# Kernel optimization log

Measured on AMD Instinct MI355X. Metric: run time of the kernel, lower is better.

## Reference

```python
import jax, jax.numpy as jnp
import numpy as np

N_NODES = 500000
N_EDGES = 5000000
EMBD = 16
BN_EPS = 1e-5


def setup_inputs() -> dict:
    key = jax.random.key(0)
    ks = jax.random.split(key, 16)
    d = EMBD
    s = 0.25  # param scale ~ 1/sqrt(d)
    inp = {
        "x": jax.random.normal(ks[0], (N_NODES, d), jnp.float32),
        "edge_index": jax.random.randint(ks[1], (2, N_EDGES), 0, N_NODES, jnp.int64 if jax.config.jax_enable_x64 else jnp.int32),
        "edge_attr": jax.random.normal(ks[2], (N_EDGES, d), jnp.float32),
        # ResGatedGraphConv params (torch Linear math: y = x @ W + b, W stored (in,out))
        "Wk": jax.random.normal(ks[3], (d, d), jnp.float32) * s,
        "bk": jax.random.normal(ks[4], (d,), jnp.float32) * s,
        "Wq": jax.random.normal(ks[5], (d, d), jnp.float32) * s,
        "bq": jax.random.normal(ks[6], (d,), jnp.float32) * s,
        "Wv": jax.random.normal(ks[7], (d, d), jnp.float32) * s,
        "bv": jax.random.normal(ks[8], (d,), jnp.float32) * s,
        "We": jax.random.normal(ks[9], (d, d), jnp.float32) * s,   # lin_edge, no bias
        "Ws": jax.random.normal(ks[10], (d, d), jnp.float32) * s,  # lin_skip (root weight)
        "bs": jax.random.normal(ks[11], (d,), jnp.float32) * s,
        "bias": jax.random.normal(ks[12], (d,), jnp.float32) * s,  # conv output bias
        # BatchNorm1d affine params
        "gamma": jnp.ones((d,), jnp.float32),
        "beta": jnp.zeros((d,), jnp.float32),
    }
    return inp


def reference(x, edge_index, edge_attr, Wk, bk, Wq, bq, Wv, bv, We, Ws, bs, bias, gamma, beta):
    # --- ResGatedGraphConv (PyG semantics, act=sigmoid, root_weight=True) ---
    src = edge_index[0]  # j (source)
    tgt = edge_index[1]  # i (target, aggregation index)
    k = x @ Wk + bk      # lin_key(x_i side)   [N, d]
    q = x @ Wq + bq      # lin_query(x_j side) [N, d]
    v = x @ Wv + bv      # lin_value(x_j side) [N, d]
    e = edge_attr @ We   # lin_edge (bias=False) [E, d]
    # message: sigmoid(k_i + e_ij + q_j) * v_j
    gate = jax.nn.sigmoid(k[tgt] + e + q[src])
    msg = gate * v[src]  # [E, d]
    agg = jax.ops.segment_sum(msg, tgt, num_segments=N_NODES)  # scatter-add to targets
    h = agg + (x @ Ws + bs) + bias  # root skip + conv bias
    # --- BatchNorm1d (training mode: batch statistics over node dim) ---
    mean = jnp.mean(h, axis=0)
    var = jnp.mean(jnp.square(h - mean), axis=0)  # biased variance
    h = (h - mean) * jax.lax.rsqrt(var + BN_EPS) * gamma + beta
    # --- ReLU + residual ---
    h = jax.nn.relu(h)
    return x + h
```

## Files before the change

### kernel.cpp

```cpp
#include <hip/hip_runtime.h>
#include <hip/hip_bf16.h>
#include <hip/hip_fp16.h>

#define D 16

typedef _Float16 f16x4 __attribute__((ext_vector_type(4)));
typedef float f32x4 __attribute__((ext_vector_type(4)));

__global__ void node_prep(const float* __restrict__ x,
                          const float* __restrict__ Wk, const float* __restrict__ bk,
                          const float* __restrict__ Wq, const float* __restrict__ bq,
                          const float* __restrict__ Wv, const float* __restrict__ bv,
                          const float* __restrict__ Ws, const float* __restrict__ bs,
                          const float* __restrict__ bias,
                          __half* __restrict__ k_h, __half* __restrict__ qv_h,
                          float* __restrict__ skip, int n_nodes) {
    __shared__ float sWk[D * D], sWq[D * D], sWv[D * D], sWs[D * D], sb[4 * D];
    for (int i = threadIdx.x; i < D * D; i += blockDim.x) {
        sWk[i] = Wk[i]; sWq[i] = Wq[i]; sWv[i] = Wv[i]; sWs[i] = Ws[i];
    }
    if (threadIdx.x < D) {
        sb[threadIdx.x]         = bk[threadIdx.x];
        sb[D + threadIdx.x]     = bq[threadIdx.x];
        sb[2 * D + threadIdx.x] = bv[threadIdx.x];
        sb[3 * D + threadIdx.x] = bs[threadIdx.x] + bias[threadIdx.x];
    }
    __syncthreads();
    int n = blockIdx.x * blockDim.x + threadIdx.x;
    if (n >= n_nodes) return;

    float xr[D];
    const float4* xp = (const float4*)(x + (size_t)n * D);
#pragma unroll
    for (int i = 0; i < 4; i++) {
        float4 t = xp[i];
        xr[4*i] = t.x; xr[4*i+1] = t.y; xr[4*i+2] = t.z; xr[4*i+3] = t.w;
    }
    float kr[D], qr[D], vr[D], hr[D];
#pragma unroll
    for (int c = 0; c < D; c++) {
        kr[c] = sb[c]; qr[c] = sb[D + c]; vr[c] = sb[2*D + c]; hr[c] = sb[3*D + c];
    }
#pragma unroll
    for (int j = 0; j < D; j++) {
        float xj = xr[j];
#pragma unroll
        for (int c = 0; c < D; c++) {
            kr[c] = fmaf(xj, sWk[j * D + c], kr[c]);
            qr[c] = fmaf(xj, sWq[j * D + c], qr[c]);
            vr[c] = fmaf(xj, sWv[j * D + c], vr[c]);
            hr[c] = fmaf(xj, sWs[j * D + c], hr[c]);
        }
    }
    __align__(16) __half2 kp[8];
#pragma unroll
    for (int i = 0; i < 8; i++) kp[i] = __floats2half2_rn(kr[2*i], kr[2*i+1]);
    float4* kd = (float4*)(k_h + (size_t)n * D);
    kd[0] = *(float4*)&kp[0];
    kd[1] = *(float4*)&kp[4];
    __align__(16) __half2 qp[16];
#pragma unroll
    for (int i = 0; i < 8; i++) qp[i]     = __floats2half2_rn(qr[2*i], qr[2*i+1]);
#pragma unroll
    for (int i = 0; i < 8; i++) qp[8 + i] = __floats2half2_rn(vr[2*i], vr[2*i+1]);
    float4* qd = (float4*)(qv_h + (size_t)n * 32);
#pragma unroll
    for (int i = 0; i < 4; i++) qd[i] = *(float4*)&qp[4*i];
    float4* sp = (float4*)(skip + (size_t)n * D);
#pragma unroll
    for (int i = 0; i < 4; i++)
        sp[i] = make_float4(hr[4*i], hr[4*i+1], hr[4*i+2], hr[4*i+3]);
}

__global__ void edge_msg_mfma(const int* __restrict__ ei, const float* __restrict__ ea,
                              const float* __restrict__ We,
                              const __half* __restrict__ k_h,
                              const __half* __restrict__ qv_h,
                              __half* __restrict__ hagg,
                              int n_edges) {
    __shared__ __align__(16) int ssrc[64];
    __shared__ __align__(16) int stgt[64];
    int lane = threadIdx.x & 63;
    int wv = threadIdx.x >> 6;
    int c = lane & 15;
    int g = lane >> 4;

    f16x4 bfrag;
#pragma unroll
    for (int i = 0; i < 4; i++) bfrag[i] = (_Float16)We[(4*g + i) * D + c];

    long long blockbase = (long long)blockIdx.x * 64;
    {
        int t = threadIdx.x;
        if (t < 64) {
            long long e = blockbase + t;
            ssrc[t] = (e < n_edges) ? __builtin_nontemporal_load(&ei[e]) : 0;
        } else if (t < 128) {
            long long e = blockbase + (t - 64);
            stgt[t - 64] = (e < n_edges) ? __builtin_nontemporal_load(&ei[(size_t)n_edges + e]) : 0;
        }
    }
    __syncthreads();

    long long wbase = blockbase + (long long)wv * 16;
    if (wbase >= n_edges) return;

    long long arow = wbase + c;
    if (arow >= n_edges) arow = n_edges - 1;
    const float* ap = ea + (size_t)arow * D + 4 * g;
    float av0 = __builtin_nontemporal_load(ap + 0);
    float av1 = __builtin_nontemporal_load(ap + 1);
    float av2 = __builtin_nontemporal_load(ap + 2);
    float av3 = __builtin_nontemporal_load(ap + 3);
    f16x4 afrag = { (_Float16)av0, (_Float16)av1, (_Float16)av2, (_Float16)av3 };

    f32x4 e4 = __builtin_amdgcn_mfma_f32_16x16x16f16(afrag, bfrag, (f32x4){0.f,0.f,0.f,0.f}, 0, 0, 0);

    int le = wv * 16 + 4 * g;
    int4 src4 = *(const int4*)(ssrc + le);
    int4 tgt4 = *(const int4*)(stgt + le);
    int srcs[4] = { src4.x, src4.y, src4.z, src4.w };
    int tgts[4] = { tgt4.x, tgt4.y, tgt4.z, tgt4.w };

    float msg[4];
#pragma unroll
    for (int r = 0; r < 4; r++) {
        float kk = __half2float(k_h[(size_t)tgts[r] * D + c]);
        float qq = __half2float(qv_h[(size_t)srcs[r] * 32 + c]);
        float vv = __half2float(qv_h[(size_t)srcs[r] * 32 + D + c]);
        float z = kk + e4[r] + qq;
        msg[r] = vv / (1.f + __expf(-z));
    }

#pragma unroll
    for (int r = 0; r < 4; r++) {
        float partner = __shfl_xor(msg[r], 1);
        long long eidx = wbase + 4 * g + r;
        if (((c & 1) == 0) && eidx < n_edges) {
            __half2 m2 = __floats2half2_rn(msg[r], partner);
            unsafeAtomicAdd((__half2*)&hagg[(size_t)tgts[r] * D + c], m2);
        }
    }
}

__global__ void bn_stats(const float* __restrict__ skip, const __half* __restrict__ hagg,
                         float* __restrict__ stats, int n_nodes) {
    float s = 0.f, ss = 0.f;
    size_t total = (size_t)n_nodes * D;
    size_t stride = (size_t)gridDim.x * blockDim.x;
    for (size_t i = (size_t)blockIdx.x * blockDim.x + threadIdx.x; i < total; i += stride) {
        float val = skip[i] + __half2float(hagg[i]);
        s += val;
        ss = fmaf(val, val, ss);
    }
    s += __shfl_xor(s, 16); s += __shfl_xor(s, 32);
    ss += __shfl_xor(ss, 16); ss += __shfl_xor(ss, 32);
    __shared__ float ls[4 * D], lss[4 * D];
    int wave = threadIdx.x >> 6, lane = threadIdx.x & 63;
    if (lane < D) { ls[wave * D + lane] = s; lss[wave * D + lane] = ss; }
    __syncthreads();
    if (threadIdx.x < D) {
        float ts = 0.f, tss = 0.f;
#pragma unroll
        for (int w = 0; w < 4; w++) { ts += ls[w * D + threadIdx.x]; tss += lss[w * D + threadIdx.x]; }
        atomicAdd(&stats[threadIdx.x], ts);
        atomicAdd(&stats[D + threadIdx.x], tss);
    }
}

__global__ void bn_finalize(const float* __restrict__ x, const __half* __restrict__ hagg,
                            const float* __restrict__ stats,
                            const float* __restrict__ gamma, const float* __restrict__ beta,
                            float* __restrict__ out, int n_nodes) {
    __shared__ float sc[D], sh[D];
    if (threadIdx.x < D) {
        float inv_n = 1.f / (float)n_nodes;
        float mean = stats[threadIdx.x] * inv_n;
        float var = stats[D + threadIdx.x] * inv_n - mean * mean;
        float inv = rsqrtf(var + 1e-5f);
        float g = gamma[threadIdx.x] * inv;
        sc[threadIdx.x] = g;
        sh[threadIdx.x] = beta[threadIdx.x] - mean * g;
    }
    __syncthreads();
    size_t i = (size_t)blockIdx.x * blockDim.x + threadIdx.x;
    size_t total = (size_t)n_nodes * D;
    if (i >= total) return;
    int c = (int)(i & (D - 1));
    float h = out[i] + __half2float(hagg[i]);
    float t = fmaf(h, sc[c], sh[c]);
    out[i] = x[i] + fmaxf(t, 0.f);
}

extern "C" void kernel_launch(void* const* d_in, const int* in_sizes, int n_in,
                              void* d_out, int out_size, void* d_ws, size_t ws_size,
                              hipStream_t stream) {
    const float* x     = (const float*)d_in[0];
    const int*   ei    = (const int*)d_in[1];
    const float* ea    = (const float*)d_in[2];
    const float* Wk    = (const float*)d_in[3];
    const float* bk    = (const float*)d_in[4];
    const float* Wq    = (const float*)d_in[5];
    const float* bq    = (const float*)d_in[6];
    const float* Wv    = (const float*)d_in[7];
    const float* bv    = (const float*)d_in[8];
    const float* We    = (const float*)d_in[9];
    const float* Ws    = (const float*)d_in[10];
    const float* bs    = (const float*)d_in[11];
    const float* bias  = (const float*)d_in[12];
    const float* gamma = (const float*)d_in[13];
    const float* beta  = (const float*)d_in[14];

    int n_nodes = in_sizes[0] / D;
    int n_edges = in_sizes[1] / 2;
    float* out = (float*)d_out;

    __half* qv_h = (__half*)d_ws;
    __half* k_h  = qv_h + (size_t)n_nodes * 32;
    __half* hagg = k_h + (size_t)n_nodes * D;
    float* stats = (float*)(hagg + (size_t)n_nodes * D);

    hipMemsetAsync(hagg, 0, (size_t)n_nodes * D * sizeof(__half), stream);
    hipMemsetAsync(stats, 0, 2 * D * sizeof(float), stream);

    int nb_nodes = (n_nodes + 255) / 256;
    node_prep<<<nb_nodes, 256, 0, stream>>>(x, Wk, bk, Wq, bq, Wv, bv, Ws, bs, bias,
                                            k_h, qv_h, out, n_nodes);

    int nb_edges = (n_edges + 63) / 64;
    edge_msg_mfma<<<nb_edges, 256, 0, stream>>>(ei, ea, We, k_h, qv_h, hagg, n_edges);

    bn_stats<<<2048, 256, 0, stream>>>(out, hagg, stats, n_nodes);

    size_t total = (size_t)n_nodes * D;
    int nb_fin = (int)((total + 255) / 256);
    bn_finalize<<<nb_fin, 256, 0, stream>>>(x, hagg, stats, gamma, beta, out, n_nodes);
}
```

Measured before the change: 369.6 us.

## Store skip in fp16, fold memsets into node_prep, vectorize BN kernels by half2

The root-skip term is now stored as fp16 in a workspace buffer rather than fp32 in the output, which halves its write and read traffic. The two hipMemsetAsync calls are removed: node_prep zeroes each node's aggregation row and the stats buffer itself. bn_stats and bn_finalize now handle two channels per thread through half2 and float2 loads. The cost is extra fp16 rounding on the skip term. Zeroing stats from block 0 of node_prep relies on that kernel finishing before bn_stats runs, which stream order guarantees.

```diff
diff --git a/kernel.cpp b/kernel.cpp
--- a/kernel.cpp
+++ b/kernel.cpp
@@ -6,6 +6,7 @@
 
 typedef _Float16 f16x4 __attribute__((ext_vector_type(4)));
 typedef float f32x4 __attribute__((ext_vector_type(4)));
+
 
 __global__ void node_prep(const float* __restrict__ x,
                           const float* __restrict__ Wk, const float* __restrict__ bk,
@@ -14,7 +15,8 @@
                           const float* __restrict__ Ws, const float* __restrict__ bs,
                           const float* __restrict__ bias,
                           __half* __restrict__ k_h, __half* __restrict__ qv_h,
-                          float* __restrict__ skip, int n_nodes) {
+                          __half* __restrict__ skip_h, __half* __restrict__ hagg,
+                          float* __restrict__ stats, int n_nodes) {
     __shared__ float sWk[D * D], sWq[D * D], sWv[D * D], sWs[D * D], sb[4 * D];
     for (int i = threadIdx.x; i < D * D; i += blockDim.x) {
         sWk[i] = Wk[i]; sWq[i] = Wq[i]; sWv[i] = Wv[i]; sWs[i] = Ws[i];
@@ -25,6 +27,7 @@
         sb[2 * D + threadIdx.x] = bv[threadIdx.x];
         sb[3 * D + threadIdx.x] = bs[threadIdx.x] + bias[threadIdx.x];
     }
+    if (blockIdx.x == 0 && threadIdx.x < 2 * D) stats[threadIdx.x] = 0.f;
     __syncthreads();
     int n = blockIdx.x * blockDim.x + threadIdx.x;
     if (n >= n_nodes) return;
@@ -66,10 +69,15 @@
     float4* qd = (float4*)(qv_h + (size_t)n * 32);
 #pragma unroll
     for (int i = 0; i < 4; i++) qd[i] = *(float4*)&qp[4*i];
-    float4* sp = (float4*)(skip + (size_t)n * D);
-#pragma unroll
-    for (int i = 0; i < 4; i++)
-        sp[i] = make_float4(hr[4*i], hr[4*i+1], hr[4*i+2], hr[4*i+3]);
+    __align__(16) __half2 sp16[8];
+#pragma unroll
+    for (int i = 0; i < 8; i++) sp16[i] = __floats2half2_rn(hr[2*i], hr[2*i+1]);
+    float4* sd = (float4*)(skip_h + (size_t)n * D);
+    sd[0] = *(float4*)&sp16[0];
+    sd[1] = *(float4*)&sp16[4];
+    float4* hz = (float4*)(hagg + (size_t)n * D);
+    hz[0] = make_float4(0.f, 0.f, 0.f, 0.f);
+    hz[1] = make_float4(0.f, 0.f, 0.f, 0.f);
 }
 
 __global__ void edge_msg_mfma(const int* __restrict__ ei, const float* __restrict__ ea,
@@ -143,21 +151,30 @@
     }
 }
 
-__global__ void bn_stats(const float* __restrict__ skip, const __half* __restrict__ hagg,
+__global__ void bn_stats(const __half* __restrict__ skip_h, const __half* __restrict__ hagg,
                          float* __restrict__ stats, int n_nodes) {
-    float s = 0.f, ss = 0.f;
-    size_t total = (size_t)n_nodes * D;
+    float s0 = 0.f, s1 = 0.f, ss0 = 0.f, ss1 = 0.f;
+    size_t total2 = (size_t)n_nodes * 8;
     size_t stride = (size_t)gridDim.x * blockDim.x;
-    for (size_t i = (size_t)blockIdx.x * blockDim.x + threadIdx.x; i < total; i += stride) {
-        float val = skip[i] + __half2float(hagg[i]);
-        s += val;
-        ss = fmaf(val, val, ss);
-    }
-    s += __shfl_xor(s, 16); s += __shfl_xor(s, 32);
-    ss += __shfl_xor(ss, 16); ss += __shfl_xor(ss, 32);
+    for (size_t i = (size_t)blockIdx.x * blockDim.x + threadIdx.x; i < total2; i += stride) {
+        __half2 a = ((const __half2*)skip_h)[i];
+        __half2 b = ((const __half2*)hagg)[i];
+        float v0 = __low2float(a) + __low2float(b);
+        float v1 = __high2float(a) + __high2float(b);
+        s0 += v0; ss0 = fmaf(v0, v0, ss0);
+        s1 += v1; ss1 = fmaf(v1, v1, ss1);
+    }
+#pragma unroll
+    for (int off = 8; off < 64; off <<= 1) {
+        s0 += __shfl_xor(s0, off); s1 += __shfl_xor(s1, off);
+        ss0 += __shfl_xor(ss0, off); ss1 += __shfl_xor(ss1, off);
+    }
     __shared__ float ls[4 * D], lss[4 * D];
     int wave = threadIdx.x >> 6, lane = threadIdx.x & 63;
-    if (lane < D) { ls[wave * D + lane] = s; lss[wave * D + lane] = ss; }
+    if (lane < 8) {
+        ls[wave * D + 2 * lane] = s0;  ls[wave * D + 2 * lane + 1] = s1;
+        lss[wave * D + 2 * lane] = ss0; lss[wave * D + 2 * lane + 1] = ss1;
+    }
     __syncthreads();
     if (threadIdx.x < D) {
         float ts = 0.f, tss = 0.f;
@@ -168,7 +185,8 @@
     }
 }
 
-__global__ void bn_finalize(const float* __restrict__ x, const __half* __restrict__ hagg,
+__global__ void bn_finalize(const float* __restrict__ x,
+                            const __half* __restrict__ skip_h, const __half* __restrict__ hagg,
                             const float* __restrict__ stats,
                             const float* __restrict__ gamma, const float* __restrict__ beta,
                             float* __restrict__ out, int n_nodes) {
@@ -184,12 +202,20 @@
     }
     __syncthreads();
     size_t i = (size_t)blockIdx.x * blockDim.x + threadIdx.x;
-    size_t total = (size_t)n_nodes * D;
-    if (i >= total) return;
-    int c = (int)(i & (D - 1));
-    float h = out[i] + __half2float(hagg[i]);
-    float t = fmaf(h, sc[c], sh[c]);
-    out[i] = x[i] + fmaxf(t, 0.f);
+    size_t total2 = (size_t)n_nodes * 8;
+    if (i >= total2) return;
+    int c0 = 2 * (int)(i & 7);
+    __half2 a = ((const __half2*)skip_h)[i];
+    __half2 b = ((const __half2*)hagg)[i];
+    float2 xv = ((const float2*)x)[i];
+    float h0 = __low2float(a) + __low2float(b);
+    float h1 = __high2float(a) + __high2float(b);
+    float t0 = fmaf(h0, sc[c0], sh[c0]);
+    float t1 = fmaf(h1, sc[c0 + 1], sh[c0 + 1]);
+    float2 o;
+    o.x = xv.x + fmaxf(t0, 0.f);
+    o.y = xv.y + fmaxf(t1, 0.f);
+    ((float2*)out)[i] = o;
 }
 
 extern "C" void kernel_launch(void* const* d_in, const int* in_sizes, int n_in,
@@ -215,24 +241,22 @@
     int n_edges = in_sizes[1] / 2;
     float* out = (float*)d_out;
 
-    __half* qv_h = (__half*)d_ws;
-    __half* k_h  = qv_h + (size_t)n_nodes * 32;
-    __half* hagg = k_h + (size_t)n_nodes * D;
-    float* stats = (float*)(hagg + (size_t)n_nodes * D);
-
-    hipMemsetAsync(hagg, 0, (size_t)n_nodes * D * sizeof(__half), stream);
-    hipMemsetAsync(stats, 0, 2 * D * sizeof(float), stream);
+    __half* qv_h   = (__half*)d_ws;
+    __half* k_h    = qv_h + (size_t)n_nodes * 32;
+    __half* hagg   = k_h + (size_t)n_nodes * D;
+    __half* skip_h = hagg + (size_t)n_nodes * D;
+    float*  stats  = (float*)(skip_h + (size_t)n_nodes * D);
 
     int nb_nodes = (n_nodes + 255) / 256;
     node_prep<<<nb_nodes, 256, 0, stream>>>(x, Wk, bk, Wq, bq, Wv, bv, Ws, bs, bias,
-                                            k_h, qv_h, out, n_nodes);
+                                            k_h, qv_h, skip_h, hagg, stats, n_nodes);
 
     int nb_edges = (n_edges + 63) / 64;
     edge_msg_mfma<<<nb_edges, 256, 0, stream>>>(ei, ea, We, k_h, qv_h, hagg, n_edges);
 
-    bn_stats<<<2048, 256, 0, stream>>>(out, hagg, stats, n_nodes);
-
-    size_t total = (size_t)n_nodes * D;
-    int nb_fin = (int)((total + 255) / 256);
-    bn_finalize<<<nb_fin, 256, 0, stream>>>(x, hagg, stats, gamma, beta, out, n_nodes);
-}
+    bn_stats<<<2048, 256, 0, stream>>>(skip_h, hagg, stats, n_nodes);
+
+    size_t total2 = (size_t)n_nodes * 8;
+    int nb_fin = (int)((total2 + 255) / 256);
+    bn_finalize<<<nb_fin, 256, 0, stream>>>(x, skip_h, hagg, stats, gamma, beta, out, n_nodes);
+}
```

Result: faster. 352.2 us (-4.7%).
